# Performance work log

Hardware: AMD Instinct MI355X
Metric: run time of the kernel (lower is better)

The kernel has to match this reference:

```python
import jax, jax.numpy as jnp
import numpy as np

D_MODEL = 1024
NUM_HEADS = 16
D_FF = 2688
BATCH = 2
SEQ = 2048
EPS = 1e-5


def _trunc_normal(key, shape, std):
    # truncated normal on [-3, 3] then scaled by std (matches trunc_normal_(mean=0,std,a=-3,b=3) approximately)
    return std * jax.random.truncated_normal(key, -3.0 / std if std > 0 else -3.0, 3.0 / std if std > 0 else 3.0, shape, jnp.float32) * std / std if False else jax.random.truncated_normal(key, -3.0, 3.0, shape, jnp.float32) * std


def setup_inputs() -> dict:
    key = jax.random.key(0)
    ks = jax.random.split(key, 8)
    def lin(k, d_out, d_in):
        std = (2.0 / (d_in + d_out)) ** 0.5
        return _trunc_normal(k, (d_out, d_in), std)
    return {
        "x": jax.random.normal(ks[0], (BATCH, SEQ, D_MODEL), jnp.float32),
        "wqkv": lin(ks[1], 3 * D_MODEL, D_MODEL),
        "wo": lin(ks[2], D_MODEL, D_MODEL),
        "g1": jnp.ones((D_MODEL,), jnp.float32),
        "g2": jnp.ones((D_MODEL,), jnp.float32),
        "w1": lin(ks[3], D_FF, D_MODEL),
        "w2": lin(ks[4], D_MODEL, D_FF),
        "w3": lin(ks[5], D_FF, D_MODEL),
    }


def _rmsnorm(x, g):
    rms = jnp.sqrt(jnp.mean(x * x, axis=-1, keepdims=True) + EPS)
    return x * (g / rms)


def _mhsa(x, wqkv, wo):
    B, S, D = x.shape
    H, Dk = NUM_HEADS, D // NUM_HEADS
    qkv = jnp.einsum('bsd,ed->bse', x, wqkv)  # [B,S,3D]
    q, k, v = jnp.split(qkv, 3, axis=-1)
    def heads(t):
        return t.reshape(B, S, H, Dk).transpose(0, 2, 1, 3)  # [B,H,S,Dk]
    q, k, v = heads(q), heads(k), heads(v)
    scores = jnp.einsum('bhqd,bhkd->bhqk', q, k) / jnp.sqrt(jnp.asarray(Dk, x.dtype))
    causal = jnp.tril(jnp.ones((S, S), bool))
    scores = jnp.where(causal, scores, -jnp.inf)
    attn = jax.nn.softmax(scores, axis=-1)
    out = jnp.einsum('bhqk,bhkd->bhqd', attn, v)
    out = out.transpose(0, 2, 1, 3).reshape(B, S, D)
    return jnp.einsum('bsd,ed->bse', out, wo)


def _swiglu(x, w1, w2, w3):
    a = jnp.einsum('bsd,fd->bsf', x, w1)
    b = jnp.einsum('bsd,fd->bsf', x, w3)
    h = (a * jax.nn.sigmoid(a)) * b
    return jnp.einsum('bsf,df->bsd', h, w2)


def reference(x, wqkv, wo, g1, g2, w1, w2, w3):
    x = x + _mhsa(_rmsnorm(x, g1), wqkv, wo)
    x = x + _swiglu(_rmsnorm(x, g2), w1, w2, w3)
    return x
```

## Files before the change

kernel.cpp:

```cpp
#include <hip/hip_runtime.h>
#include <cstdint>
#include <cstddef>

typedef unsigned short u16;
typedef __attribute__((ext_vector_type(8))) short short8;
typedef __attribute__((ext_vector_type(4))) float float4v;

struct alignas(8) u16x4 { u16 x, y, z, w; };

__device__ __forceinline__ float bf2f(u16 u) {
  union { uint32_t i; float f; } x;
  x.i = ((uint32_t)u) << 16;
  return x.f;
}
__device__ __forceinline__ u16 f2bf(float f) {
  union { float f; uint32_t i; } x;
  x.f = f;
  uint32_t r = x.i + 0x7fffu + ((x.i >> 16) & 1u);
  return (u16)(r >> 16);
}
__device__ __forceinline__ int4 pack8(const float4& a, const float4& b) {
  int4 r;
  r.x = (uint32_t)f2bf(a.x) | ((uint32_t)f2bf(a.y) << 16);
  r.y = (uint32_t)f2bf(a.z) | ((uint32_t)f2bf(a.w) << 16);
  r.z = (uint32_t)f2bf(b.x) | ((uint32_t)f2bf(b.y) << 16);
  r.w = (uint32_t)f2bf(b.z) | ((uint32_t)f2bf(b.w) << 16);
  return r;
}

__device__ __forceinline__ void gload_lds16(const void* g, void* l) {
  __builtin_amdgcn_global_load_lds(
      (const __attribute__((address_space(1))) void*)g,
      (__attribute__((address_space(3))) void*)l, 16, 0, 0);
}

struct PrepArgs {
  const float* src[5];
  u16* dst[5];
  int pre[6];
};

__global__ __launch_bounds__(256) void prep_kernel(PrepArgs a)
{
  const int g = blockIdx.x * 256 + threadIdx.x;
  if (g >= a.pre[5]) return;
  int t = 0;
#pragma unroll
  for (int i = 0; i < 5; i++) if (g >= a.pre[i + 1]) t = i + 1;
  const int idx = (g - a.pre[t]) * 8;
  const float* s = a.src[t] + idx;
  float4 v0 = *(const float4*)(s);
  float4 v1 = *(const float4*)(s + 4);
  *(int4*)(a.dst[t] + idx) = pack8(v0, v1);
}

template <int RMODE, bool OUTF32, int TN>
__global__ __launch_bounds__(256) void gemm_bt_kernel(
    const u16* __restrict__ A, const u16* __restrict__ B,
    void* __restrict__ Cv, const void* __restrict__ Rv,
    int M, int N, int K)
{
  constexpr int JN = TN / 32;
  __shared__ u16 As[128 * 32];
  __shared__ u16 Bs[TN * 32];
  const int t = threadIdx.x;
  const int lane = t & 63;
  const int wave = t >> 6;
  const int l15 = lane & 15;
  const int quad = lane >> 4;
  const int wm = (wave >> 1) * 64;
  const int wn = (wave & 1) * (TN / 2);
  const int m0 = blockIdx.y * 128;
  const int n0 = blockIdx.x * TN;
  const int sw = quad ^ ((l15 >> 1) & 3);

  float4v acc[4][JN] = {};

  const int r0 = t >> 2, q0s = (t & 3) ^ ((t >> 3) & 3);
  const int s1 = 256 + t;
  const int r1 = s1 >> 2, q1s = (s1 & 3) ^ ((s1 >> 3) & 3);

  for (int kk = 0; kk < K; kk += 32) {
    gload_lds16(A + (size_t)(m0 + r0) * K + kk + q0s * 8, &As[(wave * 64) * 8]);
    gload_lds16(A + (size_t)(m0 + r1) * K + kk + q1s * 8, &As[(256 + wave * 64) * 8]);
    gload_lds16(B + (size_t)(n0 + r0) * K + kk + q0s * 8, &Bs[(wave * 64) * 8]);
    if (TN == 128)
      gload_lds16(B + (size_t)(n0 + r1) * K + kk + q1s * 8, &Bs[(256 + wave * 64) * 8]);
    __syncthreads();
    short8 af[4], bf[JN];
#pragma unroll
    for (int i = 0; i < 4; i++)
      af[i] = *(const short8*)(&As[((wm + i * 16 + l15) * 4 + sw) * 8]);
#pragma unroll
    for (int j = 0; j < JN; j++)
      bf[j] = *(const short8*)(&Bs[((wn + j * 16 + l15) * 4 + sw) * 8]);
#pragma unroll
    for (int i = 0; i < 4; i++)
#pragma unroll
      for (int j = 0; j < JN; j++)
        acc[i][j] = __builtin_amdgcn_mfma_f32_16x16x32_bf16(af[i], bf[j], acc[i][j], 0, 0, 0);
    __syncthreads();
  }

#pragma unroll
  for (int i = 0; i < 4; i++) {
#pragma unroll
    for (int r = 0; r < 4; r++) {
      const int row = m0 + wm + i * 16 + quad * 4 + r;
      const size_t base = (size_t)row * N;
#pragma unroll
      for (int j = 0; j < JN; j++) {
        const int col = n0 + wn + j * 16 + l15;
        float v = acc[i][j][r];
        if (RMODE == 1) v += ((const float*)Rv)[base + col];
        if (RMODE == 2) v += bf2f(((const u16*)Rv)[base + col]);
        if (OUTF32) ((float*)Cv)[base + col] = v;
        else        ((u16*)Cv)[base + col] = f2bf(v);
      }
    }
  }
}

__global__ __launch_bounds__(256) void gemm_w13_kernel(
    const u16* __restrict__ A, const u16* __restrict__ B1,
    const u16* __restrict__ B2, u16* __restrict__ C,
    int M, int N, int K)
{
  __shared__ u16 As[128 * 32];
  __shared__ u16 B1s[64 * 32];
  __shared__ u16 B2s[64 * 32];
  const int t = threadIdx.x;
  const int lane = t & 63;
  const int wave = t >> 6;
  const int l15 = lane & 15;
  const int quad = lane >> 4;
  const int wm = (wave >> 1) * 64;
  const int wn = (wave & 1) * 32;
  const int m0 = blockIdx.y * 128;
  const int n0 = blockIdx.x * 64;
  const int sw = quad ^ ((l15 >> 1) & 3);

  float4v accA[4][2] = {};
  float4v accB[4][2] = {};

  const int r0 = t >> 2, q0s = (t & 3) ^ ((t >> 3) & 3);
  const int s1 = 256 + t;
  const int r1 = s1 >> 2, q1s = (s1 & 3) ^ ((s1 >> 3) & 3);

  for (int kk = 0; kk < K; kk += 32) {
    gload_lds16(A + (size_t)(m0 + r0) * K + kk + q0s * 8, &As[(wave * 64) * 8]);
    gload_lds16(A + (size_t)(m0 + r1) * K + kk + q1s * 8, &As[(256 + wave * 64) * 8]);
    gload_lds16(B1 + (size_t)(n0 + r0) * K + kk + q0s * 8, &B1s[(wave * 64) * 8]);
    gload_lds16(B2 + (size_t)(n0 + r0) * K + kk + q0s * 8, &B2s[(wave * 64) * 8]);
    __syncthreads();
    short8 af[4], b1f[2], b2f[2];
#pragma unroll
    for (int i = 0; i < 4; i++)
      af[i] = *(const short8*)(&As[((wm + i * 16 + l15) * 4 + sw) * 8]);
#pragma unroll
    for (int j = 0; j < 2; j++) {
      b1f[j] = *(const short8*)(&B1s[((wn + j * 16 + l15) * 4 + sw) * 8]);
      b2f[j] = *(const short8*)(&B2s[((wn + j * 16 + l15) * 4 + sw) * 8]);
    }
#pragma unroll
    for (int i = 0; i < 4; i++)
#pragma unroll
      for (int j = 0; j < 2; j++) {
        accA[i][j] = __builtin_amdgcn_mfma_f32_16x16x32_bf16(af[i], b1f[j], accA[i][j], 0, 0, 0);
        accB[i][j] = __builtin_amdgcn_mfma_f32_16x16x32_bf16(af[i], b2f[j], accB[i][j], 0, 0, 0);
      }
    __syncthreads();
  }

#pragma unroll
  for (int i = 0; i < 4; i++) {
#pragma unroll
    for (int r = 0; r < 4; r++) {
      const int row = m0 + wm + i * 16 + quad * 4 + r;
      const size_t base = (size_t)row * N;
#pragma unroll
      for (int j = 0; j < 2; j++) {
        const int col = n0 + wn + j * 16 + l15;
        float a = accA[i][j][r];
        float b = accB[i][j][r];
        float h = a / (1.f + __expf(-a)) * b;
        C[base + col] = f2bf(h);
      }
    }
  }
}

__global__ __launch_bounds__(256) void vtrans_kernel(
    const u16* __restrict__ qkv, u16* __restrict__ VtG)
{
  __shared__ u16 T[64 * 72];
  const int t = threadIdx.x;
  const int s0 = blockIdx.x * 64;
  const int bh = blockIdx.y, b = bh >> 4, h = bh & 15;
  {
    const int sl = t >> 2, dseg = (t & 3) * 16;
    const size_t src = ((size_t)b * 2048 + s0 + sl) * 3072 + 2048 + h * 64 + dseg;
    int4 v0 = *(const int4*)(qkv + src);
    int4 v1 = *(const int4*)(qkv + src + 8);
    *(int4*)(&T[sl * 72 + dseg]) = v0;
    *(int4*)(&T[sl * 72 + dseg + 8]) = v1;
  }
  __syncthreads();
  {
    const int d = t >> 2, sseg = (t & 3) * 16;
    alignas(16) u16 buf[16];
#pragma unroll
    for (int i = 0; i < 16; i++) buf[i] = T[(sseg + i) * 72 + d];
    u16* dst = VtG + ((size_t)bh * 64 + d) * 2048 + s0 + sseg;
    *(int4*)(dst) = *(const int4*)(&buf[0]);
    *(int4*)(dst + 8) = *(const int4*)(&buf[8]);
  }
}

__global__ __launch_bounds__(256) void attn_kernel(
    const u16* __restrict__ qkv, const u16* __restrict__ VtG,
    u16* __restrict__ outp)
{
  __shared__ u16 Ks[2][128 * 32];
  __shared__ u16 Vt[4][64 * 32];
  __shared__ u16 Pl[4][2048];
  const int t = threadIdx.x;
  const int lane = t & 63;
  const int wave = t >> 6;
  const int l15 = lane & 15;
  const int quad = lane >> 4;
  const int sw = quad ^ ((l15 >> 1) & 3);
  const int pair = blockIdx.x;
  const int bh = blockIdx.y;
  const int b = bh >> 4, h = bh & 15;
  const size_t srow = (size_t)b * 2048;
  const int rr = lane >> 2, qs = (lane & 3) ^ ((lane >> 3) & 3);
  u16* plw = Pl[wave];

  for (int tsel = 0; tsel < 2; tsel++) {
    const int qt = tsel ? 31 - pair : pair;
    const int tq0 = qt * 64;
    const int q = tq0 + wave * 16 + l15;

    short8 qf[2];
    {
      const size_t qbase = (srow + q) * 3072 + h * 64;
#pragma unroll
      for (int dh = 0; dh < 2; dh++) {
        int4 raw = *(const int4*)(qkv + qbase + dh * 32 + quad * 8);
        const u16* rp = (const u16*)&raw;
        short8 f;
#pragma unroll
        for (int j = 0; j < 8; j++)
          ((u16*)&f)[j] = f2bf(bf2f(rp[j]) * 0.125f);
        qf[dh] = f;
      }
    }

    float m_i = -INFINITY, l_i = 0.f;
    float4v accO[4] = {};
    const int nc = (qt + 2) >> 1;

    for (int ic = 0; ic < nc; ic++) {
      const int c0 = ic * 128;
#pragma unroll
      for (int k = 0; k < 8; k++) {
        const int I = wave * 8 + k;
        if (I < 16) {
          const int half = I >> 3, rb = (I & 7) * 16, row = rb + rr;
          gload_lds16(qkv + (srow + c0 + row) * 3072 + 1024 + h * 64 + half * 32 + qs * 8,
                      &Ks[half][rb * 32]);
        } else {
          const int g = (I - 16) >> 2, rb = ((I - 16) & 3) * 16, row = rb + rr;
          gload_lds16(VtG + ((size_t)bh * 64 + row) * 2048 + c0 + g * 32 + qs * 8,
                      &Vt[g][rb * 32]);
        }
      }
      __syncthreads();

      float4v accS[8];
#pragma unroll
      for (int ks = 0; ks < 8; ks++) {
        short8 kf0 = *(const short8*)(&Ks[0][((ks * 16 + l15) * 4 + sw) * 8]);
        short8 kf1 = *(const short8*)(&Ks[1][((ks * 16 + l15) * 4 + sw) * 8]);
        float4v z = {};
        z = __builtin_amdgcn_mfma_f32_16x16x32_bf16(kf0, qf[0], z, 0, 0, 0);
        accS[ks] = __builtin_amdgcn_mfma_f32_16x16x32_bf16(kf1, qf[1], z, 0, 0, 0);
      }

      if (ic == nc - 1) {
#pragma unroll
        for (int ks = 0; ks < 8; ks++)
#pragma unroll
          for (int r = 0; r < 4; r++)
            if (c0 + ks * 16 + quad * 4 + r > q) accS[ks][r] = -INFINITY;
      }

      float cmax = -INFINITY;
#pragma unroll
      for (int ks = 0; ks < 8; ks++)
#pragma unroll
        for (int r = 0; r < 4; r++) cmax = fmaxf(cmax, accS[ks][r]);
      cmax = fmaxf(cmax, __shfl_xor(cmax, 16));
      cmax = fmaxf(cmax, __shfl_xor(cmax, 32));
      const float mn = fmaxf(m_i, cmax);
      const float alpha = __expf(m_i - mn);

      float psum = 0.f;
#pragma unroll
      for (int ks = 0; ks < 8; ks++) {
        float p0 = __expf(accS[ks][0] - mn);
        float p1 = __expf(accS[ks][1] - mn);
        float p2 = __expf(accS[ks][2] - mn);
        float p3 = __expf(accS[ks][3] - mn);
        psum += (p0 + p1) + (p2 + p3);
        u16x4 pk;
        pk.x = f2bf(p0); pk.y = f2bf(p1); pk.z = f2bf(p2); pk.w = f2bf(p3);
        const int seg = ((ks & 1) * 2 + (quad >> 1)) ^ ((l15 >> 1) & 3);
        *(u16x4*)(&plw[(ks >> 1) * 512 + (l15 * 4 + seg) * 8 + (quad & 1) * 4]) = pk;
      }
      psum += __shfl_xor(psum, 16);
      psum += __shfl_xor(psum, 32);
      l_i = l_i * alpha + psum;
      m_i = mn;
#pragma unroll
      for (int ds = 0; ds < 4; ds++)
#pragma unroll
        for (int r = 0; r < 4; r++) accO[ds][r] *= alpha;

      __threadfence_block();

#pragma unroll
      for (int kh = 0; kh < 4; kh++) {
        short8 pf = *(const short8*)(&plw[kh * 512 + (l15 * 4 + sw) * 8]);
#pragma unroll
        for (int ds = 0; ds < 4; ds++) {
          short8 vf = *(const short8*)(&Vt[kh][((ds * 16 + l15) * 4 + sw) * 8]);
          accO[ds] = __builtin_amdgcn_mfma_f32_16x16x32_bf16(vf, pf, accO[ds], 0, 0, 0);
        }
      }
      __syncthreads();
    }

    const float invl = 1.f / l_i;
    const size_t obase = (srow + q) * 1024 + h * 64;
#pragma unroll
    for (int ds = 0; ds < 4; ds++) {
      u16x4 pk;
      pk.x = f2bf(accO[ds][0] * invl);
      pk.y = f2bf(accO[ds][1] * invl);
      pk.z = f2bf(accO[ds][2] * invl);
      pk.w = f2bf(accO[ds][3] * invl);
      *(u16x4*)(outp + obase + ds * 16 + quad * 4) = pk;
    }
  }
}

template <bool XF32>
__global__ __launch_bounds__(256) void rmsnorm_kernel(
    const void* __restrict__ xv, const float* __restrict__ g, u16* __restrict__ o)
{
  const int row = blockIdx.x;
  const int t = threadIdx.x;
  float f0, f1, f2, f3;
  if (XF32) {
    float4 v = *(const float4*)((const float*)xv + (size_t)row * 1024 + t * 4);
    f0 = v.x; f1 = v.y; f2 = v.z; f3 = v.w;
  } else {
    int2 v = *(const int2*)((const u16*)xv + (size_t)row * 1024 + t * 4);
    const u16* p = (const u16*)&v;
    f0 = bf2f(p[0]); f1 = bf2f(p[1]); f2 = bf2f(p[2]); f3 = bf2f(p[3]);
  }
  float ss = f0 * f0 + f1 * f1 + f2 * f2 + f3 * f3;
#pragma unroll
  for (int off = 32; off > 0; off >>= 1) ss += __shfl_down(ss, off);
  __shared__ float red[4];
  if ((t & 63) == 0) red[t >> 6] = ss;
  __syncthreads();
  const float tot = red[0] + red[1] + red[2] + red[3];
  const float inv = rsqrtf(tot * (1.0f / 1024.0f) + 1e-5f);
  float4 gv = *(const float4*)(g + t * 4);
  u16x4 ov;
  ov.x = f2bf(f0 * gv.x * inv);
  ov.y = f2bf(f1 * gv.y * inv);
  ov.z = f2bf(f2 * gv.z * inv);
  ov.w = f2bf(f3 * gv.w * inv);
  *(u16x4*)(o + (size_t)row * 1024 + t * 4) = ov;
}

extern "C" void kernel_launch(void* const* d_in, const int* in_sizes, int n_in,
                              void* d_out, int out_size, void* d_ws, size_t ws_size,
                              hipStream_t stream)
{
  const float* x    = (const float*)d_in[0];
  const float* wqkv = (const float*)d_in[1];
  const float* wo   = (const float*)d_in[2];
  const float* g1   = (const float*)d_in[3];
  const float* g2   = (const float*)d_in[4];
  const float* w1   = (const float*)d_in[5];
  const float* w2   = (const float*)d_in[6];
  const float* w3   = (const float*)d_in[7];
  float* out = (float*)d_out;
  char* ws = (char*)d_ws;
  (void)in_sizes; (void)n_in; (void)out_size; (void)ws_size;

  size_t off = 0;
  auto alloc = [&](size_t bytes) { void* p = ws + off; off += (bytes + 255) & ~(size_t)255; return p; };
  u16* wqkvb = (u16*)alloc((size_t)3072 * 1024 * 2);
  u16* wob   = (u16*)alloc((size_t)1024 * 1024 * 2);
  u16* w1b   = (u16*)alloc((size_t)2688 * 1024 * 2);
  u16* w2b   = (u16*)alloc((size_t)2688 * 1024 * 2);
  u16* w3b   = (u16*)alloc((size_t)2688 * 1024 * 2);
  u16* S1    = (u16*)alloc((size_t)4096 * 1024 * 2);
  u16* S2    = (u16*)alloc((size_t)4096 * 3072 * 2);
  u16* S3    = (u16*)alloc((size_t)4096 * 1024 * 2);
  u16* VtG   = (u16*)alloc((size_t)32 * 64 * 2048 * 2);

  PrepArgs pa;
  const float* srcs[5] = {wqkv, wo, w1, w2, w3};
  u16* dsts[5] = {wqkvb, wob, w1b, w2b, w3b};
  const int nelem[5] = {3072 * 1024, 1024 * 1024, 2688 * 1024, 2688 * 1024, 2688 * 1024};
  int pre = 0;
  for (int i = 0; i < 5; i++) {
    pa.src[i] = srcs[i];
    pa.dst[i] = dsts[i];
    pa.pre[i] = pre;
    pre += nelem[i] / 8;
  }
  pa.pre[5] = pre;
  prep_kernel<<<(pre + 255) / 256, 256, 0, stream>>>(pa);

  rmsnorm_kernel<true><<<4096, 256, 0, stream>>>(x, g1, S1);
  gemm_bt_kernel<0, false, 128><<<dim3(24, 32), 256, 0, stream>>>(S1, wqkvb, S2,
                                                  nullptr, 4096, 3072, 1024);
  vtrans_kernel<<<dim3(32, 32), 256, 0, stream>>>(S2, VtG);
  attn_kernel<<<dim3(16, 32), 256, 0, stream>>>(S2, VtG, S1);
  gemm_bt_kernel<1, false, 64><<<dim3(16, 32), 256, 0, stream>>>(S1, wob, S3, x,
                                                  4096, 1024, 1024);
  rmsnorm_kernel<false><<<4096, 256, 0, stream>>>(S3, g2, S1);
  gemm_w13_kernel<<<dim3(42, 32), 256, 0, stream>>>(S1, w1b, w3b, S2,
                                                  4096, 2688, 1024);
  gemm_bt_kernel<2, true, 64><<<dim3(16, 32), 256, 0, stream>>>(S2, w2b, out, S3,
                                                  4096, 1024, 2688);
}
```

Measured before the change: 352.3 us.

## Double-buffer GEMM LDS tiles and add XCD-aware block swizzle

Both GEMM kernels now use two LDS buffers, so the global-to-LDS load of the next K slice is issued before the MFMAs on the current slice, with the loop unrolled by two. A block-index remap groups consecutive workgroups onto the same XCD, applied to the GEMMs and to the attention kernel, to improve L2 reuse of shared A/B tiles and K/V. The cost is doubled LDS per block, which may lower occupancy. The loop also assumes K is a multiple of 64, and the remap assumes the workgroup count is divisible by 8.

Result: faster. 339.6 us (-3.6%).

```diff
diff --git a/kernel.cpp b/kernel.cpp
--- a/kernel.cpp
+++ b/kernel.cpp
@@ -34,6 +34,16 @@
       (__attribute__((address_space(3))) void*)l, 16, 0, 0);
 }
 
+__device__ __forceinline__ int2 xcd_swizzle_xmajor() {
+  const int gx = gridDim.x, gy = gridDim.y;
+  const int nwg = gx * gy;
+  const int lin = blockIdx.x + blockIdx.y * gx;
+  const int nl = (lin & 7) * (nwg >> 3) + (lin >> 3);
+  const int bx = nl / gy;
+  const int by = nl - bx * gy;
+  return make_int2(bx, by);
+}
+
 struct PrepArgs {
   const float* src[5];
   u16* dst[5];
@@ -61,8 +71,8 @@
     int M, int N, int K)
 {
   constexpr int JN = TN / 32;
-  __shared__ u16 As[128 * 32];
-  __shared__ u16 Bs[TN * 32];
+  __shared__ u16 As[2][128 * 32];
+  __shared__ u16 Bs[2][TN * 32];
   const int t = threadIdx.x;
   const int lane = t & 63;
   const int wave = t >> 6;
@@ -70,8 +80,9 @@
   const int quad = lane >> 4;
   const int wm = (wave >> 1) * 64;
   const int wn = (wave & 1) * (TN / 2);
-  const int m0 = blockIdx.y * 128;
-  const int n0 = blockIdx.x * TN;
+  const int2 bb = xcd_swizzle_xmajor();
+  const int m0 = bb.y * 128;
+  const int n0 = bb.x * TN;
   const int sw = quad ^ ((l15 >> 1) & 3);
 
   float4v acc[4][JN] = {};
@@ -80,25 +91,36 @@
   const int s1 = 256 + t;
   const int r1 = s1 >> 2, q1s = (s1 & 3) ^ ((s1 >> 3) & 3);
 
-  for (int kk = 0; kk < K; kk += 32) {
-    gload_lds16(A + (size_t)(m0 + r0) * K + kk + q0s * 8, &As[(wave * 64) * 8]);
-    gload_lds16(A + (size_t)(m0 + r1) * K + kk + q1s * 8, &As[(256 + wave * 64) * 8]);
-    gload_lds16(B + (size_t)(n0 + r0) * K + kk + q0s * 8, &Bs[(wave * 64) * 8]);
+  auto stage = [&](int bi, int kk) {
+    gload_lds16(A + (size_t)(m0 + r0) * K + kk + q0s * 8, &As[bi][(wave * 64) * 8]);
+    gload_lds16(A + (size_t)(m0 + r1) * K + kk + q1s * 8, &As[bi][(256 + wave * 64) * 8]);
+    gload_lds16(B + (size_t)(n0 + r0) * K + kk + q0s * 8, &Bs[bi][(wave * 64) * 8]);
     if (TN == 128)
-      gload_lds16(B + (size_t)(n0 + r1) * K + kk + q1s * 8, &Bs[(256 + wave * 64) * 8]);
+      gload_lds16(B + (size_t)(n0 + r1) * K + kk + q1s * 8, &Bs[bi][(256 + wave * 64) * 8]);
+  };
+  auto compute = [&](int bi) {
+    short8 af[4], bfr[JN];
+#pragma unroll
+    for (int i = 0; i < 4; i++)
+      af[i] = *(const short8*)(&As[bi][((wm + i * 16 + l15) * 4 + sw) * 8]);
+#pragma unroll
+    for (int j = 0; j < JN; j++)
+      bfr[j] = *(const short8*)(&Bs[bi][((wn + j * 16 + l15) * 4 + sw) * 8]);
+#pragma unroll
+    for (int i = 0; i < 4; i++)
+#pragma unroll
+      for (int j = 0; j < JN; j++)
+        acc[i][j] = __builtin_amdgcn_mfma_f32_16x16x32_bf16(af[i], bfr[j], acc[i][j], 0, 0, 0);
+  };
+
+  stage(0, 0);
+  __syncthreads();
+  for (int kk = 0; kk < K; kk += 64) {
+    stage(1, kk + 32);
+    compute(0);
     __syncthreads();
-    short8 af[4], bf[JN];
-#pragma unroll
-    for (int i = 0; i < 4; i++)
-      af[i] = *(const short8*)(&As[((wm + i * 16 + l15) * 4 + sw) * 8]);
-#pragma unroll
-    for (int j = 0; j < JN; j++)
-      bf[j] = *(const short8*)(&Bs[((wn + j * 16 + l15) * 4 + sw) * 8]);
-#pragma unroll
-    for (int i = 0; i < 4; i++)
-#pragma unroll
-      for (int j = 0; j < JN; j++)
-        acc[i][j] = __builtin_amdgcn_mfma_f32_16x16x32_bf16(af[i], bf[j], acc[i][j], 0, 0, 0);
+    if (kk + 64 < K) stage(0, kk + 64);
+    compute(1);
     __syncthreads();
   }
 
@@ -126,9 +148,9 @@
     const u16* __restrict__ B2, u16* __restrict__ C,
     int M, int N, int K)
 {
-  __shared__ u16 As[128 * 32];
-  __shared__ u16 B1s[64 * 32];
-  __shared__ u16 B2s[64 * 32];
+  __shared__ u16 As[2][128 * 32];
+  __shared__ u16 B1s[2][64 * 32];
+  __shared__ u16 B2s[2][64 * 32];
   const int t = threadIdx.x;
   const int lane = t & 63;
   const int wave = t >> 6;
@@ -136,8 +158,9 @@
   const int quad = lane >> 4;
   const int wm = (wave >> 1) * 64;
   const int wn = (wave & 1) * 32;
-  const int m0 = blockIdx.y * 128;
-  const int n0 = blockIdx.x * 64;
+  const int2 bb = xcd_swizzle_xmajor();
+  const int m0 = bb.y * 128;
+  const int n0 = bb.x * 64;
   const int sw = quad ^ ((l15 >> 1) & 3);
 
   float4v accA[4][2] = {};
@@ -147,20 +170,21 @@
   const int s1 = 256 + t;
   const int r1 = s1 >> 2, q1s = (s1 & 3) ^ ((s1 >> 3) & 3);
 
-  for (int kk = 0; kk < K; kk += 32) {
-    gload_lds16(A + (size_t)(m0 + r0) * K + kk + q0s * 8, &As[(wave * 64) * 8]);
-    gload_lds16(A + (size_t)(m0 + r1) * K + kk + q1s * 8, &As[(256 + wave * 64) * 8]);
-    gload_lds16(B1 + (size_t)(n0 + r0) * K + kk + q0s * 8, &B1s[(wave * 64) * 8]);
-    gload_lds16(B2 + (size_t)(n0 + r0) * K + kk + q0s * 8, &B2s[(wave * 64) * 8]);
-    __syncthreads();
+  auto stage = [&](int bi, int kk) {
+    gload_lds16(A + (size_t)(m0 + r0) * K + kk + q0s * 8, &As[bi][(wave * 64) * 8]);
+    gload_lds16(A + (size_t)(m0 + r1) * K + kk + q1s * 8, &As[bi][(256 + wave * 64) * 8]);
+    gload_lds16(B1 + (size_t)(n0 + r0) * K + kk + q0s * 8, &B1s[bi][(wave * 64) * 8]);
+    gload_lds16(B2 + (size_t)(n0 + r0) * K + kk + q0s * 8, &B2s[bi][(wave * 64) * 8]);
+  };
+  auto compute = [&](int bi) {
     short8 af[4], b1f[2], b2f[2];
 #pragma unroll
     for (int i = 0; i < 4; i++)
-      af[i] = *(const short8*)(&As[((wm + i * 16 + l15) * 4 + sw) * 8]);
+      af[i] = *(const short8*)(&As[bi][((wm + i * 16 + l15) * 4 + sw) * 8]);
 #pragma unroll
     for (int j = 0; j < 2; j++) {
-      b1f[j] = *(const short8*)(&B1s[((wn + j * 16 + l15) * 4 + sw) * 8]);
-      b2f[j] = *(const short8*)(&B2s[((wn + j * 16 + l15) * 4 + sw) * 8]);
+      b1f[j] = *(const short8*)(&B1s[bi][((wn + j * 16 + l15) * 4 + sw) * 8]);
+      b2f[j] = *(const short8*)(&B2s[bi][((wn + j * 16 + l15) * 4 + sw) * 8]);
     }
 #pragma unroll
     for (int i = 0; i < 4; i++)
@@ -169,6 +193,16 @@
         accA[i][j] = __builtin_amdgcn_mfma_f32_16x16x32_bf16(af[i], b1f[j], accA[i][j], 0, 0, 0);
         accB[i][j] = __builtin_amdgcn_mfma_f32_16x16x32_bf16(af[i], b2f[j], accB[i][j], 0, 0, 0);
       }
+  };
+
+  stage(0, 0);
+  __syncthreads();
+  for (int kk = 0; kk < K; kk += 64) {
+    stage(1, kk + 32);
+    compute(0);
+    __syncthreads();
+    if (kk + 64 < K) stage(0, kk + 64);
+    compute(1);
     __syncthreads();
   }
 
@@ -230,8 +264,12 @@
   const int l15 = lane & 15;
   const int quad = lane >> 4;
   const int sw = quad ^ ((l15 >> 1) & 3);
-  const int pair = blockIdx.x;
-  const int bh = blockIdx.y;
+  const int gx = gridDim.x;
+  const int nwg = gx * gridDim.y;
+  const int lin = blockIdx.x + blockIdx.y * gx;
+  const int nl = (lin & 7) * (nwg >> 3) + (lin >> 3);
+  const int bh = nl / gx;
+  const int pair = nl - bh * gx;
   const int b = bh >> 4, h = bh & 15;
   const size_t srow = (size_t)b * 2048;
   const int rr = lane >> 2, qs = (lane & 3) ^ ((lane >> 3) & 3);
```
